# Optimization experiments

Measured on AMD Instinct MI355X. Metric: run time of the kernel, lower is better.

## Reference

```python
import jax, jax.numpy as jnp
import numpy as np

IN, OUT, RANK, ALPHA, GS = 4096, 4096, 16, 32, 64
SCALING = ALPHA / RANK  # alpha / rank = 2.0


def setup_inputs() -> dict:
    key = jax.random.key(0)
    k1, k2, k3, k4, k5 = jax.random.split(key, 5)
    x = jax.random.normal(k1, (4, 2048, IN), dtype=jnp.float32)
    # signed int4 codes in [-8, 7]
    q_w = jax.random.randint(k2, (OUT, IN), -8, 8, dtype=jnp.int32)
    # per-group absmax scales (positive, small)
    scales = jax.random.uniform(k3, (OUT, IN // GS), dtype=jnp.float32) * 0.02 + 1e-3
    lora_A = jax.random.normal(k4, (RANK, IN), dtype=jnp.float32) * 0.02
    lora_B = jax.random.normal(k5, (OUT, RANK), dtype=jnp.float32) * 0.02
    return {"x": x, "q_w": q_w, "scales": scales, "lora_A": lora_A, "lora_B": lora_B}


def reference(x, q_w, scales, lora_A, lora_B):
    # Dequantize 4-bit base weight: blockwise symmetric, group_size=GS along in_features.
    # W[o, g*GS + j] = q[o, g*GS + j] * scales[o, g]
    W = (q_w.astype(jnp.float32).reshape(OUT, IN // GS, GS)
         * scales[:, :, None]).reshape(OUT, IN)
    # Frozen base layer: y = x @ W^T (Linear4bit, no bias)
    base_output = jnp.einsum('bsi,oi->bso', x, W)
    # LoRA branch (dropout p=0 -> identity): B(A(x)) * (alpha/rank)
    lora_output = jnp.einsum('bsr,or->bso', jnp.einsum('bsi,ri->bsr', x, lora_A), lora_B) * SCALING
    return base_output + lora_output
```

## Files before the change

### kernel.cpp

```cpp
#include <hip/hip_runtime.h>
#include <hip/hip_bf16.h>


typedef unsigned short u16;
typedef __attribute__((ext_vector_type(8))) short bf16x8;
typedef __attribute__((ext_vector_type(4))) float f32x4;
typedef __attribute__((ext_vector_type(4))) int i32x4;

#define M_DIM 8192
#define N_DIM 4096
#define K_DIM 4096
#define BK 64
#define KT_MAIN 64
#define NT 65

__device__ static inline u16 f2bf(float f) {
    union { float f; unsigned u; } v; v.f = f;
    unsigned r = v.u + 0x7fffu + ((v.u >> 16) & 1u);
    return (u16)(r >> 16);
}

__device__ static inline void gload16(const void* g, void* s) {
    __builtin_amdgcn_global_load_lds(
        (const __attribute__((address_space(1))) void*)g,
        (__attribute__((address_space(3))) void*)s, 16, 0, 0);
}

__global__ __launch_bounds__(256) void wprep_kernel(
        const int* __restrict__ q, const float* __restrict__ scales,
        u16* __restrict__ Wb) {
    int idx = blockIdx.x * 256 + threadIdx.x;
    int o  = idx >> 9;
    int kc = (idx & 511) << 3;
    float s = scales[(o << 6) + (kc >> 6)];
    const i32x4* qp = (const i32x4*)(q + (size_t)o * K_DIM + kc);
    i32x4 q0 = __builtin_nontemporal_load(qp);
    i32x4 q1 = __builtin_nontemporal_load(qp + 1);
    ushort4 r0, r1;
    r0.x = f2bf((float)q0.x * s); r0.y = f2bf((float)q0.y * s);
    r0.z = f2bf((float)q0.z * s); r0.w = f2bf((float)q0.w * s);
    r1.x = f2bf((float)q1.x * s); r1.y = f2bf((float)q1.y * s);
    r1.z = f2bf((float)q1.z * s); r1.w = f2bf((float)q1.w * s);
    *(ushort4*)&Wb[(size_t)o * K_DIM + kc]     = r0;
    *(ushort4*)&Wb[(size_t)o * K_DIM + kc + 4] = r1;
}

__global__ __launch_bounds__(256) void bprep_kernel(
        const float* __restrict__ lora_B, u16* __restrict__ B2) {
    int idx = blockIdx.x * 256 + threadIdx.x;
    int o = idx >> 6, r = idx & 63;
    B2[idx] = (r < 16) ? f2bf(lora_B[o * 16 + r]) : (u16)0;
}

__global__ __launch_bounds__(256) void xprep_kernel(
        const float* __restrict__ x, const float* __restrict__ lora_A,
        u16* __restrict__ xb, u16* __restrict__ t2) {
    const int tid = threadIdx.x, w = tid >> 6, l = tid & 63;
    const int rb = blockIdx.x * 8 + w * 2;
    float acc[2][16];
#pragma unroll
    for (int j = 0; j < 2; ++j)
#pragma unroll
        for (int r = 0; r < 16; ++r) acc[j][r] = 0.f;

    for (int i = 0; i < 16; ++i) {
        int k0 = i * 256 + l * 4;
        f32x4 x0 = __builtin_nontemporal_load(
                        (const f32x4*)&x[(size_t)rb * K_DIM + k0]);
        f32x4 x1 = __builtin_nontemporal_load(
                        (const f32x4*)&x[(size_t)(rb + 1) * K_DIM + k0]);
        ushort4 o0, o1;
        o0.x = f2bf(x0.x); o0.y = f2bf(x0.y); o0.z = f2bf(x0.z); o0.w = f2bf(x0.w);
        o1.x = f2bf(x1.x); o1.y = f2bf(x1.y); o1.z = f2bf(x1.z); o1.w = f2bf(x1.w);
        *(ushort4*)&xb[(size_t)rb * K_DIM + k0]       = o0;
        *(ushort4*)&xb[(size_t)(rb + 1) * K_DIM + k0] = o1;
#pragma unroll
        for (int r = 0; r < 16; ++r) {
            f32x4 av = *(const f32x4*)&lora_A[(size_t)r * K_DIM + k0];
            acc[0][r] += x0.x * av.x + x0.y * av.y + x0.z * av.z + x0.w * av.w;
            acc[1][r] += x1.x * av.x + x1.y * av.y + x1.z * av.z + x1.w * av.w;
        }
    }
#pragma unroll
    for (int j = 0; j < 2; ++j)
#pragma unroll
        for (int r = 0; r < 16; ++r) {
            float v = acc[j][r];
            v += __shfl_xor(v, 32); v += __shfl_xor(v, 16);
            v += __shfl_xor(v, 8);  v += __shfl_xor(v, 4);
            v += __shfl_xor(v, 2);  v += __shfl_xor(v, 1);
            acc[j][r] = v;
        }
    float lo = 0.f, hi = 0.f;
#pragma unroll
    for (int j = 0; j < 2; ++j)
#pragma unroll
        for (int c = 0; c < 8; ++c)
            if (l == j * 32 + c) { lo = acc[j][2 * c]; hi = acc[j][2 * c + 1]; }
    unsigned pack = (unsigned)f2bf(2.0f * lo) | ((unsigned)f2bf(2.0f * hi) << 16);
    *(unsigned*)&t2[(size_t)(rb + (l >> 5)) * 64 + (l & 31) * 2] = pack;
}

__global__ __launch_bounds__(512, 2) void qlora_gemm(
        const u16* __restrict__ xb, const u16* __restrict__ Wb,
        const u16* __restrict__ t2, const u16* __restrict__ B2,
        float* __restrict__ out) {
    __shared__ u16 lds[2][32768];
    int bid = blockIdx.x;
    int swz = (bid & 7) * 64 + (bid >> 3);
    int bn = swz >> 5;
    int bm = swz & 31;
    const int tid = threadIdx.x, w = tid >> 6, l = tid & 63;
    const int wr = w >> 2, wc = w & 3;
    const int fr = l & 15, fq = l >> 4;
    const int s0 = fq ^ (fr & 7);

    const int sw16 = ((l & 7) ^ ((l >> 3) & 7)) << 4;
    const int rl   = w * 8 + (l >> 3);
    const int rA0  = bm * 256 + rl;
    const int rB0  = bn * 256 + rl;
    char* ldsC = (char*)&lds[0][0];
    const int dst = w * 1024 + l * 16;

    const int arow = (wr * 128 + fr) * 128;
    const int brow = 32768 + (wc * 64 + fr) * 128;

    f32x4 acc[8][4] = {};

    auto stage = [&](int kt, int buf) {
        char* base = ldsC + buf * 65536;
        if (kt < KT_MAIN) {
            size_t ko = (size_t)kt * 128;
#pragma unroll
            for (int o = 0; o < 4; ++o) {
                gload16((const char*)xb + ((size_t)(rA0 + o * 64) * 8192 + sw16) + ko,
                        base + dst + o * 8192);
                gload16((const char*)Wb + ((size_t)(rB0 + o * 64) * 8192 + sw16) + ko,
                        base + 32768 + dst + o * 8192);
            }
        } else {
#pragma unroll
            for (int o = 0; o < 4; ++o) {
                gload16((const char*)t2 + ((size_t)(rA0 + o * 64) * 128 + sw16),
                        base + dst + o * 8192);
                gload16((const char*)B2 + ((size_t)(rB0 + o * 64) * 128 + sw16),
                        base + 32768 + dst + o * 8192);
            }
        }
    };

    stage(0, 0);
    asm volatile("s_waitcnt vmcnt(0)" ::: "memory");
    __builtin_amdgcn_s_barrier();
    asm volatile("" ::: "memory");

    bf16x8 a0[8], b0[4], a1[8], b1[4];
#pragma unroll
    for (int j = 0; j < 4; ++j)
        b0[j] = *(const bf16x8*)(ldsC + brow + j * 2048 + s0 * 16);
#pragma unroll
    for (int i = 0; i < 8; ++i)
        a0[i] = *(const bf16x8*)(ldsC + arow + i * 2048 + s0 * 16);

    for (int t = 0; t < NT; ++t) {
        const char* cb = ldsC + (t & 1) * 65536;

#pragma unroll
        for (int j = 0; j < 4; ++j)
            b1[j] = *(const bf16x8*)(cb + brow + j * 2048 + (s0 ^ 4) * 16);
#pragma unroll
        for (int i = 0; i < 8; ++i)
            a1[i] = *(const bf16x8*)(cb + arow + i * 2048 + (s0 ^ 4) * 16);
        if (t + 1 < NT) stage(t + 1, (t + 1) & 1);
        __builtin_amdgcn_sched_barrier(0);

        __builtin_amdgcn_s_setprio(1);
#pragma unroll
        for (int i = 0; i < 8; ++i)
#pragma unroll
            for (int j = 0; j < 4; ++j)
                acc[i][j] = __builtin_amdgcn_mfma_f32_16x16x32_bf16(
                                a0[i], b0[j], acc[i][j], 0, 0, 0);
        __builtin_amdgcn_s_setprio(0);
        __builtin_amdgcn_sched_barrier(0);

        asm volatile("s_waitcnt lgkmcnt(0)" ::: "memory");
        asm volatile("s_waitcnt vmcnt(0)" ::: "memory");
        __builtin_amdgcn_s_barrier();
        asm volatile("" ::: "memory");

        if (t + 1 < NT) {
            const char* nb = ldsC + ((t + 1) & 1) * 65536;
#pragma unroll
            for (int j = 0; j < 4; ++j)
                b0[j] = *(const bf16x8*)(nb + brow + j * 2048 + s0 * 16);
#pragma unroll
            for (int i = 0; i < 8; ++i)
                a0[i] = *(const bf16x8*)(nb + arow + i * 2048 + s0 * 16);
        }
        __builtin_amdgcn_sched_barrier(0);

        __builtin_amdgcn_s_setprio(1);
#pragma unroll
        for (int i = 0; i < 8; ++i)
#pragma unroll
            for (int j = 0; j < 4; ++j)
                acc[i][j] = __builtin_amdgcn_mfma_f32_16x16x32_bf16(
                                a1[i], b1[j], acc[i][j], 0, 0, 0);
        __builtin_amdgcn_s_setprio(0);
        __builtin_amdgcn_sched_barrier(0);
    }

    float* obase = out + (size_t)(bm * 256 + wr * 128 + fq * 4) * N_DIM
                       + bn * 256 + wc * 64 + fr;
#pragma unroll
    for (int i = 0; i < 8; ++i)
#pragma unroll
        for (int j = 0; j < 4; ++j)
#pragma unroll
            for (int r = 0; r < 4; ++r)
                obase[(size_t)(i * 16 + r) * N_DIM + j * 16] = acc[i][j][r];
}

extern "C" void kernel_launch(void* const* d_in, const int* in_sizes, int n_in,
                              void* d_out, int out_size, void* d_ws, size_t ws_size,
                              hipStream_t stream) {
    const float* x      = (const float*)d_in[0];
    const int*   qw     = (const int*)d_in[1];
    const float* scales = (const float*)d_in[2];
    const float* lora_A = (const float*)d_in[3];
    const float* lora_B = (const float*)d_in[4];
    float* out = (float*)d_out;

    char* ws = (char*)d_ws;
    u16* xb = (u16*)(ws);
    u16* Wb = (u16*)(ws + 67108864);
    u16* t2 = (u16*)(ws + 100663296);
    u16* B2 = (u16*)(ws + 101711872);

    wprep_kernel<<<8192, 256, 0, stream>>>(qw, scales, Wb);
    bprep_kernel<<<1024, 256, 0, stream>>>(lora_B, B2);
    xprep_kernel<<<1024, 256, 0, stream>>>(x, lora_A, xb, t2);
    qlora_gemm<<<dim3(512), 512, 0, stream>>>(xb, Wb, t2, B2, out);
}
```

Before: 313.3 us.

## Restructure GEMM main loop into 8-phase pipeline with half-tile staged loads

Replaces the two-phase double-buffered loop with an eight-phase schedule. Each K tile is split into 32-column halves for A and B, and each phase issues one staged global-to-LDS load, reads a register group, and runs 16 MFMAs, with barriers between phases. The LDS layout changes to 64-byte rows with a new XOR swizzle, and the last LoRA tile is handled in an epilogue. The aim is finer-grained overlap of global loads, LDS reads and MFMA work with lower register pressure. The cost is many more barriers per tile and careful vmcnt accounting that could break correctness.

```diff
diff --git a/kernel.cpp b/kernel.cpp
--- a/kernel.cpp
+++ b/kernel.cpp
@@ -113,102 +113,118 @@
     const int tid = threadIdx.x, w = tid >> 6, l = tid & 63;
     const int wr = w >> 2, wc = w & 3;
     const int fr = l & 15, fq = l >> 4;
-    const int s0 = fq ^ (fr & 7);
-
-    const int sw16 = ((l & 7) ^ ((l >> 3) & 7)) << 4;
-    const int rl   = w * 8 + (l >> 3);
-    const int rA0  = bm * 256 + rl;
-    const int rB0  = bn * 256 + rl;
+    const int slotSw = (fr >> 1) & 3;
+
+    const int rowStage = w * 16 + (l >> 2);
+    const int sw16 = (((l & 3) ^ ((l >> 3) & 3)) << 4);
+    const int dstStage = w * 1024 + l * 16;
     char* ldsC = (char*)&lds[0][0];
-    const int dst = w * 1024 + l * 16;
-
-    const int arow = (wr * 128 + fr) * 128;
-    const int brow = 32768 + (wc * 64 + fr) * 128;
+
+    const int aoffH = (wr * 128 + fr) * 64 + ((fq ^ slotSw) << 4);
+    const int boffH = 32768 + (wc * 64 + fr) * 64 + ((fq ^ slotSw) << 4);
 
     f32x4 acc[8][4] = {};
-
-    auto stage = [&](int kt, int buf) {
-        char* base = ldsC + buf * 65536;
+    bf16x8 ra[4], ra2[4], rbf[4];
+
+    auto stage_half = [&](int kt, int hid) {
+        if (kt >= NT) return;
+        int isB = ((hid & 1) == 0);
+        int h = hid >> 1;
+        char* dstR = ldsC + (kt & 1) * 65536 + (isB ? 32768 : 0) + h * 16384;
+        int baseRow = (isB ? bn : bm) * 256 + rowStage;
         if (kt < KT_MAIN) {
-            size_t ko = (size_t)kt * 128;
-#pragma unroll
-            for (int o = 0; o < 4; ++o) {
-                gload16((const char*)xb + ((size_t)(rA0 + o * 64) * 8192 + sw16) + ko,
-                        base + dst + o * 8192);
-                gload16((const char*)Wb + ((size_t)(rB0 + o * 64) * 8192 + sw16) + ko,
-                        base + 32768 + dst + o * 8192);
-            }
+            const char* src = isB ? (const char*)Wb : (const char*)xb;
+            size_t so = (size_t)baseRow * 8192 + (size_t)kt * 128 + h * 64 + sw16;
+            gload16(src + so, dstR + dstStage);
+            gload16(src + so + (size_t)128 * 8192, dstR + dstStage + 8192);
         } else {
-#pragma unroll
-            for (int o = 0; o < 4; ++o) {
-                gload16((const char*)t2 + ((size_t)(rA0 + o * 64) * 128 + sw16),
-                        base + dst + o * 8192);
-                gload16((const char*)B2 + ((size_t)(rB0 + o * 64) * 128 + sw16),
-                        base + 32768 + dst + o * 8192);
-            }
+            const char* src = isB ? (const char*)B2 : (const char*)t2;
+            size_t so = (size_t)baseRow * 128 + h * 64 + sw16;
+            gload16(src + so, dstR + dstStage);
+            gload16(src + so + 128 * 128, dstR + dstStage + 8192);
         }
     };
 
-    stage(0, 0);
+    auto readG = [&](const char* cb, int g) {
+        int h16 = (g >= 2) ? 16384 : 0;
+        if ((g & 1) == 0) {
+#pragma unroll
+            for (int j = 0; j < 4; ++j)
+                rbf[j] = *(const bf16x8*)(cb + boffH + h16 + j * 1024);
+#pragma unroll
+            for (int i = 0; i < 4; ++i)
+                ra[i] = *(const bf16x8*)(cb + aoffH + h16 + i * 1024);
+        } else {
+#pragma unroll
+            for (int i = 0; i < 4; ++i)
+                ra2[i] = *(const bf16x8*)(cb + aoffH + h16 + (i + 4) * 1024);
+        }
+    };
+
+    auto mfmaG = [&](int g) {
+        if ((g & 1) == 0) {
+#pragma unroll
+            for (int i = 0; i < 4; ++i)
+#pragma unroll
+                for (int j = 0; j < 4; ++j)
+                    acc[i][j] = __builtin_amdgcn_mfma_f32_16x16x32_bf16(
+                                    ra[i], rbf[j], acc[i][j], 0, 0, 0);
+        } else {
+#pragma unroll
+            for (int i = 0; i < 4; ++i)
+#pragma unroll
+                for (int j = 0; j < 4; ++j)
+                    acc[i + 4][j] = __builtin_amdgcn_mfma_f32_16x16x32_bf16(
+                                        ra2[i], rbf[j], acc[i + 4][j], 0, 0, 0);
+        }
+    };
+
+#pragma unroll
+    for (int h = 0; h < 4; ++h) stage_half(0, h);
+#pragma unroll
+    for (int h = 0; h < 3; ++h) stage_half(1, h);
+    asm volatile("s_waitcnt vmcnt(6)" ::: "memory");
+    __builtin_amdgcn_s_barrier();
+    asm volatile("" ::: "memory");
+
+    for (int it = 0; it < 32; ++it) {
+        const char* cb0 = ldsC;
+        const char* cb1 = ldsC + 65536;
+#pragma unroll
+        for (int p = 0; p < 8; ++p) {
+            const char* cb = (p < 4) ? cb0 : cb1;
+            int g = p & 3;
+            int tcur = 2 * it + (p < 4 ? 0 : 1);
+            int skt  = (g == 0) ? tcur + 1 : tcur + 2;
+            int shid = (g + 3) & 3;
+            if (g == 0)
+                asm volatile("s_waitcnt vmcnt(6)" ::: "memory");
+            readG(cb, g);
+            stage_half(skt, shid);
+            __builtin_amdgcn_sched_barrier(0);
+            __builtin_amdgcn_s_barrier();
+            asm volatile("s_waitcnt lgkmcnt(0)" ::: "memory");
+            __builtin_amdgcn_sched_barrier(0);
+            __builtin_amdgcn_s_setprio(1);
+            mfmaG(g);
+            __builtin_amdgcn_s_setprio(0);
+            __builtin_amdgcn_sched_barrier(0);
+            __builtin_amdgcn_s_barrier();
+        }
+    }
+
     asm volatile("s_waitcnt vmcnt(0)" ::: "memory");
     __builtin_amdgcn_s_barrier();
     asm volatile("" ::: "memory");
-
-    bf16x8 a0[8], b0[4], a1[8], b1[4];
-#pragma unroll
-    for (int j = 0; j < 4; ++j)
-        b0[j] = *(const bf16x8*)(ldsC + brow + j * 2048 + s0 * 16);
-#pragma unroll
-    for (int i = 0; i < 8; ++i)
-        a0[i] = *(const bf16x8*)(ldsC + arow + i * 2048 + s0 * 16);
-
-    for (int t = 0; t < NT; ++t) {
-        const char* cb = ldsC + (t & 1) * 65536;
-
-#pragma unroll
-        for (int j = 0; j < 4; ++j)
-            b1[j] = *(const bf16x8*)(cb + brow + j * 2048 + (s0 ^ 4) * 16);
-#pragma unroll
-        for (int i = 0; i < 8; ++i)
-            a1[i] = *(const bf16x8*)(cb + arow + i * 2048 + (s0 ^ 4) * 16);
-        if (t + 1 < NT) stage(t + 1, (t + 1) & 1);
-        __builtin_amdgcn_sched_barrier(0);
-
-        __builtin_amdgcn_s_setprio(1);
-#pragma unroll
-        for (int i = 0; i < 8; ++i)
-#pragma unroll
-            for (int j = 0; j < 4; ++j)
-                acc[i][j] = __builtin_amdgcn_mfma_f32_16x16x32_bf16(
-                                a0[i], b0[j], acc[i][j], 0, 0, 0);
-        __builtin_amdgcn_s_setprio(0);
-        __builtin_amdgcn_sched_barrier(0);
-
-        asm volatile("s_waitcnt lgkmcnt(0)" ::: "memory");
-        asm volatile("s_waitcnt vmcnt(0)" ::: "memory");
-        __builtin_amdgcn_s_barrier();
-        asm volatile("" ::: "memory");
-
-        if (t + 1 < NT) {
-            const char* nb = ldsC + ((t + 1) & 1) * 65536;
-#pragma unroll
-            for (int j = 0; j < 4; ++j)
-                b0[j] = *(const bf16x8*)(nb + brow + j * 2048 + s0 * 16);
-#pragma unroll
-            for (int i = 0; i < 8; ++i)
-                a0[i] = *(const bf16x8*)(nb + arow + i * 2048 + s0 * 16);
-        }
-        __builtin_amdgcn_sched_barrier(0);
-
-        __builtin_amdgcn_s_setprio(1);
-#pragma unroll
-        for (int i = 0; i < 8; ++i)
-#pragma unroll
-            for (int j = 0; j < 4; ++j)
-                acc[i][j] = __builtin_amdgcn_mfma_f32_16x16x32_bf16(
-                                a1[i], b1[j], acc[i][j], 0, 0, 0);
-        __builtin_amdgcn_s_setprio(0);
-        __builtin_amdgcn_sched_barrier(0);
+    {
+        const char* cb = ldsC;
+#pragma unroll
+        for (int g = 0; g < 4; ++g) {
+            readG(cb, g);
+            asm volatile("s_waitcnt lgkmcnt(0)" ::: "memory");
+            __builtin_amdgcn_sched_barrier(0);
+            mfmaG(g);
+        }
     }
 
     float* obase = out + (size_t)(bm * 256 + wr * 128 + fq * 4) * N_DIM
```

Result: slower. 331.3 us (+5.8%).
